# Optimization experiments

Measured on AMD Instinct MI355X. Metric: run time of the kernel, lower is better.

Reference implementation:

```python
import jax, jax.numpy as jnp
import numpy as np
from jax import lax

D_MODEL = 640
D_INNER = 1280
D_STATE = 34
D_CONV = 4
DT_RANK = 40  # ceil(640/16)
DT_MIN, DT_MAX = 1e-3, 1e-1
NUM_LAYERS = 8
BATCH, SEQ = 2, 2048


def setup_inputs() -> dict:
    key = jax.random.key(0)
    ks = jax.random.split(key, 8)
    hidden_states = jax.random.normal(ks[0], (BATCH, SEQ, D_MODEL), dtype=jnp.float32)
    W_in = jax.random.normal(ks[1], (2 * D_INNER, D_MODEL), dtype=jnp.float32) * 0.02
    conv_w = jax.random.normal(ks[2], (D_INNER, D_CONV), dtype=jnp.float32) * 0.2
    conv_b = jnp.zeros((D_INNER,), dtype=jnp.float32)
    W_x = jax.random.normal(ks[3], (DT_RANK + 2 * D_STATE, D_INNER), dtype=jnp.float32) * 0.02
    W_dt = jax.random.normal(ks[4], (D_INNER, DT_RANK), dtype=jnp.float32) * 0.02
    # dt bias init: inverse-softplus of dt sampled log-uniform in [dt_min, dt_max]
    u = jax.random.uniform(ks[5], (D_INNER,), dtype=jnp.float32)
    dt_vals = jnp.exp(u * (np.log(DT_MAX) - np.log(DT_MIN)) + np.log(DT_MIN))
    dt_bias = dt_vals + jnp.log(-jnp.expm1(-dt_vals))
    A_log = jnp.log(jnp.tile(jnp.arange(1, D_STATE + 1, dtype=jnp.float32)[None, :], (D_INNER, 1)))
    D_skip = jnp.ones((D_INNER,), dtype=jnp.float32)
    W_out = jax.random.normal(ks[6], (D_MODEL, D_INNER), dtype=jnp.float32) * (0.02 / np.sqrt(2.0 * NUM_LAYERS))
    return {"hidden_states": hidden_states, "W_in": W_in, "conv_w": conv_w,
            "conv_b": conv_b, "W_x": W_x, "W_dt": W_dt, "dt_bias": dt_bias,
            "A_log": A_log, "D_skip": D_skip, "W_out": W_out}


def _silu(v):
    return v * jax.nn.sigmoid(v)


def _causal_dwconv(x, w, b):
    # x: [B, Di, L], w: [Di, K] depthwise, left-pad K-1 for causality
    out = lax.conv_general_dilated(
        x, w[:, None, :], window_strides=(1,), padding=[(D_CONV - 1, 0)],
        feature_group_count=D_INNER, dimension_numbers=("NCH", "OIH", "NCH"))
    return out + b[None, :, None]


def _selective_scan(u, dt_sp, A, Bm, Cm):
    # u, dt_sp: [B, Di, L]; A: [Di, N]; Bm, Cm: [B, L, N]
    dtl = jnp.moveaxis(dt_sp, 2, 0)  # [L, B, Di]
    ul = jnp.moveaxis(u, 2, 0)       # [L, B, Di]

    def step(h, inp):
        dt_t, u_t, B_t, C_t = inp
        dA = jnp.exp(dt_t[..., None] * A)                   # [B, Di, N]
        h = dA * h + (dt_t * u_t)[..., None] * B_t[:, None, :]
        y = jnp.einsum("bdn,bn->bd", h, C_t)
        return h, y

    h0 = jnp.zeros((u.shape[0], D_INNER, D_STATE), dtype=u.dtype)
    _, ys = lax.scan(step, h0, (dtl, ul, jnp.swapaxes(Bm, 0, 1), jnp.swapaxes(Cm, 0, 1)))
    return jnp.moveaxis(ys, 0, 2)  # [B, Di, L]


def reference(hidden_states, W_in, conv_w, conv_b, W_x, W_dt, dt_bias, A_log, D_skip, W_out):
    # in_proj and split into x / gate z, channels-first
    xz = hidden_states @ W_in.T                    # [B, L, 2*Di]
    x = jnp.swapaxes(xz[..., :D_INNER], 1, 2)      # [B, Di, L]
    z = jnp.swapaxes(xz[..., D_INNER:], 1, 2)      # [B, Di, L]
    # causal depthwise conv + silu
    x = _silu(_causal_dwconv(x, conv_w, conv_b))
    # input-dependent dt, B, C
    x_dbl = jnp.swapaxes(x, 1, 2) @ W_x.T          # [B, L, dt_rank + 2N]
    dt_raw = x_dbl[..., :DT_RANK]
    Bm = x_dbl[..., DT_RANK:DT_RANK + D_STATE]     # [B, L, N]
    Cm = x_dbl[..., DT_RANK + D_STATE:]            # [B, L, N]
    dt = jnp.swapaxes(dt_raw @ W_dt.T, 1, 2)       # [B, Di, L]
    dt_sp = jax.nn.softplus(dt + dt_bias[None, :, None])
    A = -jnp.exp(A_log)                            # [Di, N]
    y = _selective_scan(x, dt_sp, A, Bm, Cm)
    y = y + x * D_skip[None, :, None]
    y = y * _silu(z)
    return jnp.swapaxes(y, 1, 2) @ W_out.T         # [B, L, d_model]
```

## Files before the change

### kernel.cpp

```cpp
#include <hip/hip_runtime.h>
#include <hip/hip_bf16.h>

#define D_MODEL   640
#define D_INNER   1280
#define D_STATE   34
#define D_CONV    4
#define DT_RANK   40
#define BATCH     2
#define SEQ       2048
#define XDBL_W    (DT_RANK + 2 * D_STATE)
#define M_TOTAL   (BATCH * SEQ)
#define NCHUNK    4
#define CHLEN     (SEQ / NCHUNK)
#define NQ        (CHLEN / 4)
#define QB        4
#define RECW      68

typedef __attribute__((ext_vector_type(8))) short short8v;
typedef __attribute__((ext_vector_type(4))) short short4v;
typedef __attribute__((ext_vector_type(4))) float f32x4;

__device__ __forceinline__ void split_bf16(float x, short& hi, short& lo) {
    unsigned u  = __builtin_bit_cast(unsigned, x);
    unsigned uh = u & 0xFFFF0000u;
    hi = (short)(uh >> 16);
    float r = x - __builtin_bit_cast(float, uh);
    unsigned v = __builtin_bit_cast(unsigned, r);
    v += 0x7FFFu + ((v >> 16) & 1u);
    lo = (short)(v >> 16);
}

__device__ __forceinline__ void split4(const float4& v, short4v& h, short4v& l) {
    float xs[4] = {v.x, v.y, v.z, v.w};
    #pragma unroll
    for (int j = 0; j < 4; ++j) { short hh, ll; split_bf16(xs[j], hh, ll); h[j] = hh; l[j] = ll; }
}

template<int MODE>
__global__ __launch_bounds__(256) void gemm_mfma(
    const float* __restrict__ A, const float* __restrict__ B,
    float* __restrict__ C, int M, int N, int K, int lda, int ldb, int ldc)
{
    constexpr int BMt = 128, BKt = 32;
    constexpr int LDT = 40;
    __shared__ short Ahi[BMt * LDT], Alo[BMt * LDT];
    __shared__ short Bhi[BMt * LDT], Blo[BMt * LDT];

    const int tid  = threadIdx.x;
    const long m0  = (long)blockIdx.y * BMt;
    const long n0  = (long)blockIdx.x * BMt;
    const int wid  = tid >> 6, lane = tid & 63;
    const int wr   = (wid >> 1) * 64;
    const int wc   = (wid & 1) * 64;
    const int lrow = lane & 15;
    const int lkb  = lane >> 4;

    const bool do_silu = (MODE == 2) && (m0 >= D_INNER);

    f32x4 acc[4][4] = {};

    for (int k0 = 0; k0 < K; k0 += BKt) {
        __syncthreads();
        #pragma unroll
        for (int q = 0; q < 4; ++q) {
            int flat = tid + q * 256;
            int r  = flat >> 3;
            int f4 = (flat & 7) << 2;
            float4 va = *reinterpret_cast<const float4*>(&A[(m0 + r) * lda + k0 + f4]);
            float4 vb = *reinterpret_cast<const float4*>(&B[(n0 + r) * ldb + k0 + f4]);
            short4v ah, al, bh, bl;
            split4(va, ah, al);
            split4(vb, bh, bl);
            *reinterpret_cast<short4v*>(&Ahi[r * LDT + f4]) = ah;
            *reinterpret_cast<short4v*>(&Alo[r * LDT + f4]) = al;
            *reinterpret_cast<short4v*>(&Bhi[r * LDT + f4]) = bh;
            *reinterpret_cast<short4v*>(&Blo[r * LDT + f4]) = bl;
        }
        __syncthreads();

        short8v a_hi[4], a_lo[4], b_hi[4], b_lo[4];
        #pragma unroll
        for (int i = 0; i < 4; ++i) {
            int ar = (wr + i * 16 + lrow) * LDT + lkb * 8;
            int br = (wc + i * 16 + lrow) * LDT + lkb * 8;
            a_hi[i] = *reinterpret_cast<const short8v*>(&Ahi[ar]);
            a_lo[i] = *reinterpret_cast<const short8v*>(&Alo[ar]);
            b_hi[i] = *reinterpret_cast<const short8v*>(&Bhi[br]);
            b_lo[i] = *reinterpret_cast<const short8v*>(&Blo[br]);
        }
        #pragma unroll
        for (int i = 0; i < 4; ++i)
            #pragma unroll
            for (int j = 0; j < 4; ++j) {
                acc[i][j] = __builtin_amdgcn_mfma_f32_16x16x32_bf16(a_hi[i], b_hi[j], acc[i][j], 0, 0, 0);
                acc[i][j] = __builtin_amdgcn_mfma_f32_16x16x32_bf16(a_hi[i], b_lo[j], acc[i][j], 0, 0, 0);
                acc[i][j] = __builtin_amdgcn_mfma_f32_16x16x32_bf16(a_lo[i], b_hi[j], acc[i][j], 0, 0, 0);
            }
    }

    #pragma unroll
    for (int i = 0; i < 4; ++i) {
        long grow0 = m0 + wr + i * 16 + lkb * 4;
        #pragma unroll
        for (int j = 0; j < 4; ++j) {
            long gcol = n0 + wc + j * 16 + lrow;
            #pragma unroll
            for (int r = 0; r < 4; ++r) {
                float v = acc[i][j][r];
                if (do_silu) v = v * (1.0f / (1.0f + __expf(-v)));
                C[(grow0 + r) * ldc + gcol] = v;
            }
        }
    }
}

#define BM 64
#define BN 64
#define BK 16

template<int LAYA, int LAYB, int MODE>
__global__ __launch_bounds__(256) void gemm_tn(
    const float* __restrict__ A, const float* __restrict__ B,
    float* __restrict__ C, int M, int N, int K, int lda, int ldb, int ldc,
    const float* __restrict__ bias)
{
    __shared__ float As[BK][BM + 4];
    __shared__ float Bs[BK][BN + 4];

    const int tid = threadIdx.x;
    const int m0 = blockIdx.y * BM;
    const int n0 = blockIdx.x * BN;
    const int tx = tid & 15;
    const int ty = tid >> 4;

    float acc[4][4] = {};

    for (int k0 = 0; k0 < K; k0 += BK) {
        #pragma unroll
        for (int i = 0; i < 4; ++i) {
            int idx = tid + i * 256;
            if (LAYA == 0) {
                int r = idx >> 4;
                int c = idx & 15;
                As[c][r] = (m0 + r < M && k0 + c < K)
                         ? A[(long)(m0 + r) * lda + (k0 + c)] : 0.0f;
            } else {
                int c = idx >> 6;
                int r = idx & 63;
                As[c][r] = (m0 + r < M && k0 + c < K)
                         ? A[(long)(k0 + c) * lda + (m0 + r)] : 0.0f;
            }
            if (LAYB == 0) {
                int rb = idx >> 4;
                int cb = idx & 15;
                Bs[cb][rb] = (n0 + rb < N && k0 + cb < K)
                           ? B[(long)(n0 + rb) * ldb + (k0 + cb)] : 0.0f;
            } else {
                int cb = idx >> 6;
                int rb = idx & 63;
                Bs[cb][rb] = (n0 + rb < N && k0 + cb < K)
                           ? B[(long)(k0 + cb) * ldb + (n0 + rb)] : 0.0f;
            }
        }
        __syncthreads();

        #pragma unroll
        for (int k = 0; k < BK; ++k) {
            const float4 a4 = *reinterpret_cast<const float4*>(&As[k][ty * 4]);
            const float4 b4 = *reinterpret_cast<const float4*>(&Bs[k][tx * 4]);
            const float a_[4] = {a4.x, a4.y, a4.z, a4.w};
            const float b_[4] = {b4.x, b4.y, b4.z, b4.w};
            #pragma unroll
            for (int i = 0; i < 4; ++i)
                #pragma unroll
                for (int j = 0; j < 4; ++j)
                    acc[i][j] = fmaf(a_[i], b_[j], acc[i][j]);
        }
        __syncthreads();
    }

    #pragma unroll
    for (int i = 0; i < 4; ++i) {
        int gm = m0 + ty * 4 + i;
        if (gm >= M) continue;
        float bi = (MODE == 2) ? bias[gm] : 0.0f;
        #pragma unroll
        for (int j = 0; j < 4; ++j) {
            int gn = n0 + tx * 4 + j;
            if (gn >= N) continue;
            float v = acc[i][j];
            if (MODE == 2) {
                v += bi;
                v = (v > 15.0f) ? v : log1pf(__expf(v));
            }
            C[(long)gm * ldc + gn] = v;
        }
    }
}

__global__ __launch_bounds__(256) void gemm_splitk_T(
    const float* __restrict__ A, const float* __restrict__ B,
    float* __restrict__ Cp, int M, int N, int K, int lda, int ldb, int ldc)
{
    __shared__ float As[BK][BM + 4];
    __shared__ float Bs[BK][BN + 4];

    const int tid = threadIdx.x;
    const int m0 = blockIdx.y * BM;
    const int n0 = blockIdx.x * BN;
    const int z  = blockIdx.z;
    const int kseg = K / 4;
    const int kbeg = z * kseg;
    const int tx = tid & 15;
    const int ty = tid >> 4;

    float acc[4][4] = {};

    for (int k0 = kbeg; k0 < kbeg + kseg; k0 += BK) {
        #pragma unroll
        for (int i = 0; i < 4; ++i) {
            int idx = tid + i * 256;
            int r = idx >> 4;
            int c = idx & 15;
            As[c][r] = (m0 + r < M) ? A[(long)(m0 + r) * lda + (k0 + c)] : 0.0f;
            int cb = idx >> 6;
            int rb = idx & 63;
            Bs[cb][rb] = B[(long)(k0 + cb) * ldb + (n0 + rb)];
        }
        __syncthreads();

        #pragma unroll
        for (int k = 0; k < BK; ++k) {
            const float4 a4 = *reinterpret_cast<const float4*>(&As[k][ty * 4]);
            const float4 b4 = *reinterpret_cast<const float4*>(&Bs[k][tx * 4]);
            const float a_[4] = {a4.x, a4.y, a4.z, a4.w};
            const float b_[4] = {b4.x, b4.y, b4.z, b4.w};
            #pragma unroll
            for (int i = 0; i < 4; ++i)
                #pragma unroll
                for (int j = 0; j < 4; ++j)
                    acc[i][j] = fmaf(a_[i], b_[j], acc[i][j]);
        }
        __syncthreads();
    }

    float* Cz = Cp + (long)z * M * ldc;
    #pragma unroll
    for (int i = 0; i < 4; ++i) {
        int gm = m0 + ty * 4 + i;
        if (gm >= M) continue;
        #pragma unroll
        for (int j = 0; j < 4; ++j) {
            int gn = n0 + tx * 4 + j;
            Cz[(long)gm * ldc + gn] = acc[i][j];
        }
    }
}

__global__ __launch_bounds__(256) void reduce4_kernel(
    const float* __restrict__ part, float* __restrict__ out, int n)
{
    int i4 = (blockIdx.x * 256 + threadIdx.x) * 4;
    if (i4 >= n) return;
    float4 s0 = *reinterpret_cast<const float4*>(&part[i4]);
    float4 s1 = *reinterpret_cast<const float4*>(&part[(long)n + i4]);
    float4 s2 = *reinterpret_cast<const float4*>(&part[(long)2 * n + i4]);
    float4 s3 = *reinterpret_cast<const float4*>(&part[(long)3 * n + i4]);
    float4 r;
    r.x = (s0.x + s1.x) + (s2.x + s3.x);
    r.y = (s0.y + s1.y) + (s2.y + s3.y);
    r.z = (s0.z + s1.z) + (s2.z + s3.z);
    r.w = (s0.w + s1.w) + (s2.w + s3.w);
    *reinterpret_cast<float4*>(&out[i4]) = r;
}

__global__ __launch_bounds__(256) void conv_silu_kernel(
    const float* __restrict__ xT, const float* __restrict__ cw,
    const float* __restrict__ cb, float* __restrict__ uT)
{
    int idx = blockIdx.x * 256 + threadIdx.x;
    if (idx >= D_INNER * M_TOTAL) return;
    int bs = idx & (M_TOTAL - 1);
    int d  = idx >> 12;
    int s  = bs & (SEQ - 1);

    const float* xr = xT + idx;
    float acc = cb[d];
    #pragma unroll
    for (int k = 0; k < D_CONV; ++k) {
        int off = k - (D_CONV - 1);
        if (s + off >= 0)
            acc = fmaf(xr[off], cw[d * D_CONV + k], acc);
    }
    uT[idx] = acc * (1.0f / (1.0f + __expf(-acc)));
}

__global__ __launch_bounds__(256) void transpose_kernel(
    const float* __restrict__ in, float* __restrict__ out)
{
    __shared__ float tile[32][33];
    const int tx = threadIdx.x & 31;
    const int ty = threadIdx.x >> 5;
    const int t0 = blockIdx.x * 32;
    const int d0 = blockIdx.y * 32;

    #pragma unroll
    for (int i = 0; i < 32; i += 8)
        tile[ty + i][tx] = in[(long)(d0 + ty + i) * M_TOTAL + t0 + tx];
    __syncthreads();
    #pragma unroll
    for (int i = 0; i < 32; i += 8)
        out[(long)(t0 + ty + i) * D_INNER + d0 + tx] = tile[tx][ty + i];
}

#define DPP_ADD(X_, CTRL_) {                                                 \
        int t_ = __builtin_amdgcn_update_dpp(                                \
            0, __builtin_bit_cast(int, X_), (CTRL_), 0xf, 0xf, true);        \
        X_ += __builtin_bit_cast(float, t_);                                 \
    }

__global__ __launch_bounds__(64, 4) void scan_part1(
    const float* __restrict__ xdblT,
    const float* __restrict__ spT,
    const float* __restrict__ A_log,
    const float* __restrict__ uT,
    float* __restrict__ rec)
{
    const int cid  = blockIdx.x;
    const int bd   = cid / (NCHUNK - 1);
    const int c    = cid % (NCHUNK - 1);
    const int lane = threadIdx.x;
    const int b = bd / D_INNER;
    const int d = bd % D_INNER;
    const bool act = lane < D_STATE;

    const float A_n = act ? -__expf(A_log[d * D_STATE + lane]) : 0.0f;

    const long tbase = (long)b * SEQ + (long)c * CHLEN;
    const float* sp_p = spT + (long)d * M_TOTAL + tbase;
    const float* u_p  = uT  + (long)d * M_TOTAL + tbase;
    const float* Bp   = xdblT + (long)(act ? DT_RANK + lane : 0) * M_TOTAL + tbase;

    float h = 0.0f, P = 1.0f;

#define ST1(SPX, UX, BX) {                                                   \
        float dA = __expf((SPX) * A_n);                                      \
        h = fmaf(dA, h, ((SPX) * (UX)) * (BX));                              \
        P *= dA;                                                             \
    }

    #pragma unroll 1
    for (int q0 = 0; q0 < NQ; q0 += QB) {
        float4 SP[QB], U[QB], Bq[QB];
        #pragma unroll
        for (int i = 0; i < QB; ++i) {
            int tt = (q0 + i) * 4;
            SP[i] = *reinterpret_cast<const float4*>(&sp_p[tt]);
            U[i]  = *reinterpret_cast<const float4*>(&u_p[tt]);
            Bq[i] = *reinterpret_cast<const float4*>(&Bp[tt]);
            if (!act) Bq[i] = make_float4(0.f, 0.f, 0.f, 0.f);
        }
        #pragma unroll
        for (int i = 0; i < QB; ++i) {
            ST1(SP[i].x, U[i].x, Bq[i].x);
            ST1(SP[i].y, U[i].y, Bq[i].y);
            ST1(SP[i].z, U[i].z, Bq[i].z);
            ST1(SP[i].w, U[i].w, Bq[i].w);
        }
    }
#undef ST1

    if (act) {
        rec[(long)cid * RECW + lane]      = h;
        rec[(long)cid * RECW + 34 + lane] = P;
    }
}

__global__ __launch_bounds__(64, 4) void scan_part3(
    const float* __restrict__ gT,
    const float* __restrict__ xdblT,
    const float* __restrict__ spT,
    const float* __restrict__ A_log,
    const float* __restrict__ D_skip,
    const float* __restrict__ rec,
    float* __restrict__ uT)
{
    const int cid  = blockIdx.x;
    const int bd   = cid >> 2;
    const int c    = cid & (NCHUNK - 1);
    const int lane = threadIdx.x;
    const int b = bd / D_INNER;
    const int d = bd % D_INNER;
    const bool act = lane < D_STATE;

    const float A_n = act ? -__expf(A_log[d * D_STATE + lane]) : 0.0f;
    const float Dd  = D_skip[d];

    const long tbase = (long)b * SEQ + (long)c * CHLEN;
    const float* sp_p = spT + (long)d * M_TOTAL + tbase;
    const float* g_p  = gT  + (long)d * M_TOTAL + tbase;
    float*       u_p  = uT  + (long)d * M_TOTAL + tbase;
    const float* Bp   = xdblT + (long)(act ? DT_RANK + lane : 0) * M_TOTAL + tbase;
    const float* Cp   = xdblT + (long)(act ? DT_RANK + D_STATE + lane : 0) * M_TOTAL + tbase;

    float h = 0.0f;
    for (int cc = 0; cc < c; ++cc) {
        long rbase = (long)(bd * (NCHUNK - 1) + cc) * RECW;
        float he = act ? rec[rbase + lane]      : 0.0f;
        float Pp = act ? rec[rbase + 34 + lane] : 0.0f;
        h = fmaf(Pp, h, he);
    }

#define ST(SPX, UX, GX, BX, CX, YX) {                                        \
        float dA = __expf((SPX) * A_n);                                      \
        h = fmaf(dA, h, ((SPX) * (UX)) * (BX));                              \
        float pp = h * (CX);                                                 \
        DPP_ADD(pp, 0x111);                                  \
        DPP_ADD(pp, 0x112);                                  \
        DPP_ADD(pp, 0x114);                                  \
        DPP_ADD(pp, 0x118);                                  \
        DPP_ADD(pp, 0x142);                                \
        DPP_ADD(pp, 0x143);                                \
        YX = fmaf((UX), Dd, pp) * (GX);                                      \
    }

    #pragma unroll 1
    for (int q0 = 0; q0 < NQ; q0 += QB) {
        float4 SP[QB], U[QB], G[QB], Bq[QB], Cq[QB];
        #pragma unroll
        for (int i = 0; i < QB; ++i) {
            int tt = (q0 + i) * 4;
            SP[i] = *reinterpret_cast<const float4*>(&sp_p[tt]);
            U[i]  = *reinterpret_cast<const float4*>(&u_p[tt]);
            G[i]  = *reinterpret_cast<const float4*>(&g_p[tt]);
            Bq[i] = *reinterpret_cast<const float4*>(&Bp[tt]);
            Cq[i] = *reinterpret_cast<const float4*>(&Cp[tt]);
            if (!act) { Bq[i] = make_float4(0.f,0.f,0.f,0.f);
                        Cq[i] = make_float4(0.f,0.f,0.f,0.f); }
        }
        #pragma unroll
        for (int i = 0; i < QB; ++i) {
            float4 yq;
            ST(SP[i].x, U[i].x, G[i].x, Bq[i].x, Cq[i].x, yq.x);
            ST(SP[i].y, U[i].y, G[i].y, Bq[i].y, Cq[i].y, yq.y);
            ST(SP[i].z, U[i].z, G[i].z, Bq[i].z, Cq[i].z, yq.z);
            ST(SP[i].w, U[i].w, G[i].w, Bq[i].w, Cq[i].w, yq.w);
            if (lane == 63)
                *reinterpret_cast<float4*>(&u_p[(q0 + i) * 4]) = yq;
        }
    }
#undef ST
}

extern "C" void kernel_launch(void* const* d_in, const int* in_sizes, int n_in,
                              void* d_out, int out_size, void* d_ws, size_t ws_size,
                              hipStream_t stream)
{
    const float* hs      = (const float*)d_in[0];
    const float* W_in    = (const float*)d_in[1];
    const float* conv_w  = (const float*)d_in[2];
    const float* conv_b  = (const float*)d_in[3];
    const float* W_x     = (const float*)d_in[4];
    const float* W_dt    = (const float*)d_in[5];
    const float* dt_bias = (const float*)d_in[6];
    const float* A_log   = (const float*)d_in[7];
    const float* D_skip  = (const float*)d_in[8];
    const float* W_out   = (const float*)d_in[9];
    float* out = (float*)d_out;

    float* ws    = (float*)d_ws;
    float* xT    = ws;
    float* gT    = xT    + (size_t)D_INNER * M_TOTAL;
    float* uT    = gT    + (size_t)D_INNER * M_TOTAL;
    float* xdblT = uT    + (size_t)D_INNER * M_TOTAL;
    float* spT   = xdblT + (size_t)XDBL_W * M_TOTAL;
    float* rec   = spT   + (size_t)D_INNER * M_TOTAL;
    float* part  = xT;
    float* yN    = xT;

    dim3 blk(256);

    gemm_mfma<2><<<dim3(M_TOTAL / 128, (2 * D_INNER) / 128), blk, 0, stream>>>(
        W_in, hs, xT, 2 * D_INNER, M_TOTAL, D_MODEL, D_MODEL, D_MODEL, M_TOTAL);

    conv_silu_kernel<<<(D_INNER * M_TOTAL + 255) / 256, blk, 0, stream>>>(
        xT, conv_w, conv_b, uT);

    gemm_splitk_T<<<dim3(M_TOTAL / BN, (XDBL_W + BM - 1) / BM, 4), blk, 0, stream>>>(
        W_x, uT, part, XDBL_W, M_TOTAL, D_INNER, D_INNER, M_TOTAL, M_TOTAL);

    reduce4_kernel<<<(XDBL_W * M_TOTAL / 4 + 255) / 256, blk, 0, stream>>>(
        part, xdblT, XDBL_W * M_TOTAL);

    gemm_tn<0, 1, 2><<<dim3(M_TOTAL / BN, D_INNER / BM), blk, 0, stream>>>(
        W_dt, xdblT, spT, D_INNER, M_TOTAL, DT_RANK, DT_RANK, M_TOTAL, M_TOTAL,
        dt_bias);

    scan_part1<<<BATCH * D_INNER * (NCHUNK - 1), 64, 0, stream>>>(
        xdblT, spT, A_log, uT, rec);

    scan_part3<<<BATCH * D_INNER * NCHUNK, 64, 0, stream>>>(
        gT, xdblT, spT, A_log, D_skip, rec, uT);

    transpose_kernel<<<dim3(M_TOTAL / 32, D_INNER / 32), blk, 0, stream>>>(uT, yN);

    gemm_mfma<0><<<dim3(D_MODEL / 128, M_TOTAL / 128), blk, 0, stream>>>(
        yN, W_out, out, M_TOTAL, D_MODEL, D_INNER, D_INNER, D_INNER, D_MODEL);
}
```

Baseline: 584.3 us.

## Double-buffer scan loads and pack chunk waves into one block per channel

Both scan kernels now process one (batch, channel) pair per block, with one wave per chunk, instead of launching a separate 64-thread block for every chunk. The float4 batched loads are replaced by scalar loads in a ping-pong double buffer of depth eight, so the next group's loads are in flight while the current group's recurrence runs. The output store now happens per step from lane 63, and masking of inactive lanes moves from zeroing loaded B/C values to a multiply mask. The aim is to hide global load latency behind the serial recurrence, at the cost of more scalar load instructions, narrower stores and higher register pressure.

```diff
diff --git a/kernel.cpp b/kernel.cpp
--- a/kernel.cpp
+++ b/kernel.cpp
@@ -12,9 +12,8 @@
 #define M_TOTAL   (BATCH * SEQ)
 #define NCHUNK    4
 #define CHLEN     (SEQ / NCHUNK)
-#define NQ        (CHLEN / 4)
-#define QB        4
 #define RECW      68
+#define PF        8
 
 typedef __attribute__((ext_vector_type(8))) short short8v;
 typedef __attribute__((ext_vector_type(4))) short short4v;
@@ -319,17 +318,16 @@
         X_ += __builtin_bit_cast(float, t_);                                 \
     }
 
-__global__ __launch_bounds__(64, 4) void scan_part1(
+__global__ __launch_bounds__(192) void scan_part1(
     const float* __restrict__ xdblT,
     const float* __restrict__ spT,
     const float* __restrict__ A_log,
     const float* __restrict__ uT,
     float* __restrict__ rec)
 {
-    const int cid  = blockIdx.x;
-    const int bd   = cid / (NCHUNK - 1);
-    const int c    = cid % (NCHUNK - 1);
-    const int lane = threadIdx.x;
+    const int bd   = blockIdx.x;
+    const int c    = threadIdx.x >> 6;
+    const int lane = threadIdx.x & 63;
     const int b = bd / D_INNER;
     const int d = bd % D_INNER;
     const bool act = lane < D_STATE;
@@ -343,40 +341,46 @@
 
     float h = 0.0f, P = 1.0f;
 
-#define ST1(SPX, UX, BX) {                                                   \
-        float dA = __expf((SPX) * A_n);                                      \
-        h = fmaf(dA, h, ((SPX) * (UX)) * (BX));                              \
-        P *= dA;                                                             \
-    }
-
-    #pragma unroll 1
-    for (int q0 = 0; q0 < NQ; q0 += QB) {
-        float4 SP[QB], U[QB], Bq[QB];
-        #pragma unroll
-        for (int i = 0; i < QB; ++i) {
-            int tt = (q0 + i) * 4;
-            SP[i] = *reinterpret_cast<const float4*>(&sp_p[tt]);
-            U[i]  = *reinterpret_cast<const float4*>(&u_p[tt]);
-            Bq[i] = *reinterpret_cast<const float4*>(&Bp[tt]);
-            if (!act) Bq[i] = make_float4(0.f, 0.f, 0.f, 0.f);
-        }
-        #pragma unroll
-        for (int i = 0; i < QB; ++i) {
-            ST1(SP[i].x, U[i].x, Bq[i].x);
-            ST1(SP[i].y, U[i].y, Bq[i].y);
-            ST1(SP[i].z, U[i].z, Bq[i].z);
-            ST1(SP[i].w, U[i].w, Bq[i].w);
-        }
-    }
-#undef ST1
+    float aSP[PF], aU[PF], aB[PF];
+    float bSP[PF], bU[PF], bB[PF];
+
+#define LOADS1(SP_, U_, B_, T_) {                                           \
+        int tt = (T_); tt = (tt < CHLEN) ? tt : (CHLEN - 1);                \
+        SP_ = sp_p[tt];                                                     \
+        U_  = u_p [tt];                                                     \
+        B_  = Bp  [tt];                                                     \
+    }
+
+#define STEP1(SP_, U_, B_) {                                                \
+        float dA = __expf(SP_ * A_n);                                       \
+        h = fmaf(dA, h, (SP_ * U_) * B_);                                   \
+        P *= dA;                                                            \
+    }
+
+    #pragma unroll
+    for (int i = 0; i < PF; ++i) LOADS1(aSP[i], aU[i], aB[i], i);
+
+    for (int t0 = 0; t0 < CHLEN; t0 += 2 * PF) {
+        #pragma unroll
+        for (int i = 0; i < PF; ++i) LOADS1(bSP[i], bU[i], bB[i], t0 + PF + i);
+        #pragma unroll
+        for (int i = 0; i < PF; ++i) STEP1(aSP[i], aU[i], aB[i]);
+        #pragma unroll
+        for (int i = 0; i < PF; ++i) LOADS1(aSP[i], aU[i], aB[i], t0 + 2 * PF + i);
+        #pragma unroll
+        for (int i = 0; i < PF; ++i) STEP1(bSP[i], bU[i], bB[i]);
+    }
+#undef LOADS1
+#undef STEP1
 
     if (act) {
-        rec[(long)cid * RECW + lane]      = h;
-        rec[(long)cid * RECW + 34 + lane] = P;
-    }
-}
-
-__global__ __launch_bounds__(64, 4) void scan_part3(
+        long cid = (long)bd * (NCHUNK - 1) + c;
+        rec[cid * RECW + lane]      = h;
+        rec[cid * RECW + 34 + lane] = P;
+    }
+}
+
+__global__ __launch_bounds__(256) void scan_part3(
     const float* __restrict__ gT,
     const float* __restrict__ xdblT,
     const float* __restrict__ spT,
@@ -385,16 +389,16 @@
     const float* __restrict__ rec,
     float* __restrict__ uT)
 {
-    const int cid  = blockIdx.x;
-    const int bd   = cid >> 2;
-    const int c    = cid & (NCHUNK - 1);
-    const int lane = threadIdx.x;
+    const int bd   = blockIdx.x;
+    const int c    = threadIdx.x >> 6;
+    const int lane = threadIdx.x & 63;
     const int b = bd / D_INNER;
     const int d = bd % D_INNER;
     const bool act = lane < D_STATE;
 
     const float A_n = act ? -__expf(A_log[d * D_STATE + lane]) : 0.0f;
     const float Dd  = D_skip[d];
+    const float cmask = act ? 1.0f : 0.0f;
 
     const long tbase = (long)b * SEQ + (long)c * CHLEN;
     const float* sp_p = spT + (long)d * M_TOTAL + tbase;
@@ -405,51 +409,59 @@
 
     float h = 0.0f;
     for (int cc = 0; cc < c; ++cc) {
-        long rbase = (long)(bd * (NCHUNK - 1) + cc) * RECW;
+        long rbase = ((long)bd * (NCHUNK - 1) + cc) * RECW;
         float he = act ? rec[rbase + lane]      : 0.0f;
         float Pp = act ? rec[rbase + 34 + lane] : 0.0f;
         h = fmaf(Pp, h, he);
     }
 
-#define ST(SPX, UX, GX, BX, CX, YX) {                                        \
-        float dA = __expf((SPX) * A_n);                                      \
-        h = fmaf(dA, h, ((SPX) * (UX)) * (BX));                              \
-        float pp = h * (CX);                                                 \
-        DPP_ADD(pp, 0x111);                                  \
-        DPP_ADD(pp, 0x112);                                  \
-        DPP_ADD(pp, 0x114);                                  \
-        DPP_ADD(pp, 0x118);                                  \
-        DPP_ADD(pp, 0x142);                                \
-        DPP_ADD(pp, 0x143);                                \
-        YX = fmaf((UX), Dd, pp) * (GX);                                      \
-    }
-
-    #pragma unroll 1
-    for (int q0 = 0; q0 < NQ; q0 += QB) {
-        float4 SP[QB], U[QB], G[QB], Bq[QB], Cq[QB];
-        #pragma unroll
-        for (int i = 0; i < QB; ++i) {
-            int tt = (q0 + i) * 4;
-            SP[i] = *reinterpret_cast<const float4*>(&sp_p[tt]);
-            U[i]  = *reinterpret_cast<const float4*>(&u_p[tt]);
-            G[i]  = *reinterpret_cast<const float4*>(&g_p[tt]);
-            Bq[i] = *reinterpret_cast<const float4*>(&Bp[tt]);
-            Cq[i] = *reinterpret_cast<const float4*>(&Cp[tt]);
-            if (!act) { Bq[i] = make_float4(0.f,0.f,0.f,0.f);
-                        Cq[i] = make_float4(0.f,0.f,0.f,0.f); }
-        }
-        #pragma unroll
-        for (int i = 0; i < QB; ++i) {
-            float4 yq;
-            ST(SP[i].x, U[i].x, G[i].x, Bq[i].x, Cq[i].x, yq.x);
-            ST(SP[i].y, U[i].y, G[i].y, Bq[i].y, Cq[i].y, yq.y);
-            ST(SP[i].z, U[i].z, G[i].z, Bq[i].z, Cq[i].z, yq.z);
-            ST(SP[i].w, U[i].w, G[i].w, Bq[i].w, Cq[i].w, yq.w);
-            if (lane == 63)
-                *reinterpret_cast<float4*>(&u_p[(q0 + i) * 4]) = yq;
-        }
-    }
-#undef ST
+    float aSP[PF], aU[PF], aG[PF], aB[PF], aC[PF];
+    float bSP[PF], bU[PF], bG[PF], bB[PF], bC[PF];
+
+#define LOADS(SP_, U_, G_, B_, C_, T_) {                                    \
+        int tt = (T_); tt = (tt < CHLEN) ? tt : (CHLEN - 1);                \
+        SP_ = sp_p[tt];                                                     \
+        U_  = u_p [tt];                                                     \
+        G_  = g_p [tt];                                                     \
+        B_  = Bp  [tt];                                                     \
+        C_  = Cp  [tt];                                                     \
+    }
+
+#define STEP(SP_, U_, G_, B_, C_, T_) {                                     \
+        float dA = __expf(SP_ * A_n);                                       \
+        h = fmaf(dA, h, (SP_ * U_) * B_);                                   \
+        float pp = h * C_ * cmask;                                          \
+        DPP_ADD(pp, 0x111);                                 \
+        DPP_ADD(pp, 0x112);                                 \
+        DPP_ADD(pp, 0x114);                                 \
+        DPP_ADD(pp, 0x118);                                 \
+        DPP_ADD(pp, 0x142);                               \
+        DPP_ADD(pp, 0x143);                               \
+        if (lane == 63) {                                                   \
+            float y = fmaf(U_, Dd, pp);                                     \
+            u_p[T_] = y * G_;                                               \
+        }                                                                   \
+    }
+
+    #pragma unroll
+    for (int i = 0; i < PF; ++i) LOADS(aSP[i], aU[i], aG[i], aB[i], aC[i], i);
+
+    for (int t0 = 0; t0 < CHLEN; t0 += 2 * PF) {
+        #pragma unroll
+        for (int i = 0; i < PF; ++i)
+            LOADS(bSP[i], bU[i], bG[i], bB[i], bC[i], t0 + PF + i);
+        #pragma unroll
+        for (int i = 0; i < PF; ++i)
+            STEP(aSP[i], aU[i], aG[i], aB[i], aC[i], t0 + i);
+        #pragma unroll
+        for (int i = 0; i < PF; ++i)
+            LOADS(aSP[i], aU[i], aG[i], aB[i], aC[i], t0 + 2 * PF + i);
+        #pragma unroll
+        for (int i = 0; i < PF; ++i)
+            STEP(bSP[i], bU[i], bG[i], bB[i], bC[i], t0 + PF + i);
+    }
+#undef LOADS
+#undef STEP
 }
 
 extern "C" void kernel_launch(void* const* d_in, const int* in_sizes, int n_in,
@@ -496,10 +508,10 @@
         W_dt, xdblT, spT, D_INNER, M_TOTAL, DT_RANK, DT_RANK, M_TOTAL, M_TOTAL,
         dt_bias);
 
-    scan_part1<<<BATCH * D_INNER * (NCHUNK - 1), 64, 0, stream>>>(
+    scan_part1<<<BATCH * D_INNER, 192, 0, stream>>>(
         xdblT, spT, A_log, uT, rec);
 
-    scan_part3<<<BATCH * D_INNER * NCHUNK, 64, 0, stream>>>(
+    scan_part3<<<BATCH * D_INNER, 256, 0, stream>>>(
         gT, xdblT, spT, A_log, D_skip, rec, uT);
 
     transpose_kernel<<<dim3(M_TOTAL / 32, D_INNER / 32), blk, 0, stream>>>(uT, yN);
```

New measurement: 1.115 ms. 1.91x slower.
